# Kernel tuning notes

Measured on AMD Instinct MI355X. Metric: run time of the kernel, lower is better.

Reference implementation:

```python
import jax, jax.numpy as jnp
import numpy as np

B, H, W, C = 8, 128, 128, 256
WH, WW = 8, 8            # window height/width
NH = 8                   # num heads
HD = C // NH             # head dim = 32
EPS = 1e-5


def setup_inputs() -> dict:
    key = jax.random.key(0)
    ks = jax.random.split(key, 10)
    s = 0.02
    return {
        "x": jax.random.normal(ks[0], (B, H, W, C), jnp.float32),
        "residual": jax.random.normal(ks[1], (B, H, W, C), jnp.float32),
        "ln_x_w": 1.0 + s * jax.random.normal(ks[2], (C,), jnp.float32),
        "ln_x_b": s * jax.random.normal(ks[3], (C,), jnp.float32),
        "ln_r_w": 1.0 + s * jax.random.normal(ks[4], (C,), jnp.float32),
        "ln_r_b": s * jax.random.normal(ks[5], (C,), jnp.float32),
        "in_proj_w": s * jax.random.normal(ks[6], (3 * C, C), jnp.float32),
        "in_proj_b": s * jax.random.normal(ks[7], (3 * C,), jnp.float32),
        "out_proj_w": s * jax.random.normal(ks[8], (C, C), jnp.float32),
        "out_proj_b": s * jax.random.normal(ks[9], (C,), jnp.float32),
    }


def _layernorm(t, w, b):
    m = jnp.mean(t, axis=-1, keepdims=True)
    v = jnp.var(t, axis=-1, keepdims=True)
    return (t - m) * jax.lax.rsqrt(v + EPS) * w + b


def _windows(t):
    # [B, H, W, C] -> [B * (H//WH) * (W//WW), WH*WW, C]  (non-overlapping windows)
    t = t.reshape(B, H // WH, WH, W // WW, WW, C)
    t = t.transpose(0, 1, 3, 2, 4, 5)
    return t.reshape(-1, WH * WW, C)


def _unwindows(t):
    # inverse of _windows -> [B, H, W, C]
    t = t.reshape(B, H // WH, W // WW, WH, WW, C)
    t = t.transpose(0, 1, 3, 2, 4, 5)
    return t.reshape(B, H, W, C)


def reference(x, residual, ln_x_w, ln_x_b, ln_r_w, ln_r_b,
              in_proj_w, in_proj_b, out_proj_w, out_proj_b):
    xn = _layernorm(x, ln_x_w, ln_x_b)
    rn = _layernorm(residual, ln_r_w, ln_r_b)

    q_in = _windows(xn)   # [Nw, S, C]
    kv_in = _windows(rn)  # [Nw, S, C]

    wq, wk, wv = jnp.split(in_proj_w, 3, axis=0)
    bq, bk, bv = jnp.split(in_proj_b, 3, axis=0)

    def heads(t):
        nw, s, _ = t.shape
        return t.reshape(nw, s, NH, HD).transpose(0, 2, 1, 3)  # [Nw, NH, S, HD]

    q = heads(q_in @ wq.T + bq)
    k = heads(kv_in @ wk.T + bk)
    v = heads(kv_in @ wv.T + bv)

    scale = 1.0 / jnp.sqrt(jnp.asarray(HD, q.dtype))
    scores = jnp.einsum('whqd,whkd->whqk', q, k) * scale  # [Nw, NH, S, S]
    attn = jax.nn.softmax(scores, axis=-1)
    out = jnp.einsum('whqk,whkd->whqd', attn, v)          # [Nw, NH, S, HD]
    out = out.transpose(0, 2, 1, 3).reshape(-1, WH * WW, C)
    out = out @ out_proj_w.T + out_proj_b                 # [Nw, S, C]

    return _unwindows(out)
```

## Files before the change

### kernel.cpp

```cpp
#include <hip/hip_runtime.h>
#include <math.h>

typedef unsigned int uint;
typedef unsigned short ushort;
typedef short bf16x8 __attribute__((ext_vector_type(8)));
typedef float f32x4 __attribute__((ext_vector_type(4)));

#define EPSV 1e-5f
#define SCALE 0.17677669529663687f

#define OFF_WQKV 0
#define OFF_WOUT 196608
#define OFF_BQKV 262144
#define OFF_BOUT 262912
#define OFF_LNXW 263168
#define OFF_LNXB 263424
#define OFF_LNRW 263680
#define OFF_LNRB 263936

#define L_AX 0
#define L_AR 33792
#define L_QH 67584
#define L_KH 76800
#define L_VT 86016
#define L_AO 95232
#define L_PW 129024
#define LDS_TOTAL 138240

__device__ __forceinline__ float bf2f(ushort u) {
    union { float f; uint i; } z; z.i = ((uint)u) << 16; return z.f;
}
__device__ __forceinline__ ushort f2bf(float f) {
    union { float f; uint i; } z; z.f = f;
    uint i = z.i;
    return (ushort)((i + 0x7FFFu + ((i >> 16) & 1u)) >> 16);
}
__device__ __forceinline__ uint pack2(float a, float b) {
    return (uint)f2bf(a) | ((uint)f2bf(b) << 16);
}

__device__ __forceinline__ bool detect_f32_wave(const uint* __restrict__ xw, int lane) {
    const uint e = (xw[lane] >> 7) & 0xFFu;
    const int pred = (e >= 0x60u && e <= 0x8Au) ? 1 : 0;
    const unsigned long long m = __ballot(pred);
    return __popcll(m) < 32;
}

__global__ __launch_bounds__(256) void kParams(
    const void* __restrict__ x,
    const void* __restrict__ lnxw, const void* __restrict__ lnxb,
    const void* __restrict__ lnrw, const void* __restrict__ lnrb,
    const void* __restrict__ wqkv, const void* __restrict__ bqkv,
    const void* __restrict__ wout, const void* __restrict__ bout,
    ushort* __restrict__ pb)
{
    const bool f32 = detect_f32_wave((const uint*)x, threadIdx.x & 63);
    const int blk = blockIdx.x, tid = threadIdx.x;
    const void* src; int si, doff;
    if (blk < 768)        { src = wqkv; si = blk * 256 + tid;          doff = OFF_WQKV; }
    else if (blk < 1024)  { src = wout; si = (blk - 768) * 256 + tid;  doff = OFF_WOUT; }
    else if (blk < 1027)  { src = bqkv; si = (blk - 1024) * 256 + tid; doff = OFF_BQKV; }
    else if (blk == 1027) { src = bout; si = tid; doff = OFF_BOUT; }
    else if (blk == 1028) { src = lnxw; si = tid; doff = OFF_LNXW; }
    else if (blk == 1029) { src = lnxb; si = tid; doff = OFF_LNXB; }
    else if (blk == 1030) { src = lnrw; si = tid; doff = OFF_LNRW; }
    else                  { src = lnrb; si = tid; doff = OFF_LNRB; }
    pb[doff + si] = f32 ? f2bf(((const float*)src)[si]) : ((const ushort*)src)[si];
}

__device__ __forceinline__ void loadB(const ushort* __restrict__ wbase, int wrow,
                                      int quad, bf16x8 (&bb)[8])
{
    const bf16x8* bp = (const bf16x8*)(wbase + (size_t)wrow * 256 + quad * 8);
    #pragma unroll
    for (int ks = 0; ks < 8; ++ks) bb[ks] = bp[ks * 4];
}

__device__ __forceinline__ void compT(
    const ushort* __restrict__ pb, char* __restrict__ smem,
    int t, int g, int col, int quad, const bf16x8 (&bb)[8])
{
    const int mat = t >> 2, sub = t & 3;
    const int wrow = mat * 256 + g * 64 + sub * 16 + col;
    const float bias = bf2f(pb[OFF_BQKV + wrow]);
    const ushort (*A)[264] = (const ushort (*)[264])(smem + (mat == 0 ? L_AX : L_AR));

    if (mat < 2) {
        ushort (*dst)[72] = (ushort (*)[72])(smem + (mat == 0 ? L_QH : L_KH));
        const float scl = (mat == 0) ? SCALE : 1.f;
        #pragma unroll
        for (int at = 0; at < 4; ++at) {
            f32x4 acc = {0.f, 0.f, 0.f, 0.f};
            #pragma unroll
            for (int ks = 0; ks < 8; ++ks) {
                const bf16x8 aF = *(const bf16x8*)&A[at * 16 + col][ks * 32 + quad * 8];
                acc = __builtin_amdgcn_mfma_f32_16x16x32_bf16(aF, bb[ks], acc, 0, 0, 0);
            }
            #pragma unroll
            for (int rg = 0; rg < 4; ++rg)
                dst[at * 16 + quad * 4 + rg][sub * 16 + col] = f2bf((acc[rg] + bias) * scl);
        }
    } else {
        ushort (*vT)[72] = (ushort (*)[72])(smem + L_VT);
        #pragma unroll
        for (int at = 0; at < 4; ++at) {
            f32x4 acc = {0.f, 0.f, 0.f, 0.f};
            #pragma unroll
            for (int ks = 0; ks < 8; ++ks) {
                const bf16x8 aF = *(const bf16x8*)&A[at * 16 + col][ks * 32 + quad * 8];
                acc = __builtin_amdgcn_mfma_f32_16x16x32_bf16(aF, bb[ks], acc, 0, 0, 0);
            }
            uint2 pv;
            pv.x = pack2(acc[0] + bias, acc[1] + bias);
            pv.y = pack2(acc[2] + bias, acc[3] + bias);
            *(uint2*)&vT[sub * 16 + col][at * 16 + quad * 4] = pv;
        }
    }
}

__device__ __forceinline__ void projGroup(
    const ushort* __restrict__ pb, char* __restrict__ smem,
    int g, int wave, int col, int quad)
{
    const ushort* wq = pb + OFF_WQKV;
    const int t0 = wave * 3, t1 = t0 + 1, t2 = t0 + 2;
    const int w0 = (t0 >> 2) * 256 + g * 64 + (t0 & 3) * 16 + col;
    const int w1 = (t1 >> 2) * 256 + g * 64 + (t1 & 3) * 16 + col;
    const int w2 = (t2 >> 2) * 256 + g * 64 + (t2 & 3) * 16 + col;

    bf16x8 p0[8], p1[8];
    loadB(wq, w0, quad, p0);
    loadB(wq, w1, quad, p1);
    compT(pb, smem, t0, g, col, quad, p0);
    loadB(wq, w2, quad, p0);
    compT(pb, smem, t1, g, col, quad, p1);
    compT(pb, smem, t2, g, col, quad, p0);
}

__device__ __forceinline__ void attGroup(
    char* __restrict__ smem, ushort (*Pw)[72],
    int g, int wave, int col, int quad)
{
    const ushort (*qh)[72] = (const ushort (*)[72])(smem + L_QH);
    const ushort (*kh)[72] = (const ushort (*)[72])(smem + L_KH);
    const ushort (*vT)[72] = (const ushort (*)[72])(smem + L_VT);
    ushort (*ao)[264] = (ushort (*)[264])(smem + L_AO);

    #pragma unroll
    for (int hs = 0; hs < 2; ++hs) {
        const bf16x8 qa = *(const bf16x8*)&qh[wave * 16 + col][hs * 32 + quad * 8];
        f32x4 s[4];
        #pragma unroll
        for (int nt = 0; nt < 4; ++nt) {
            const bf16x8 kb = *(const bf16x8*)&kh[nt * 16 + col][hs * 32 + quad * 8];
            f32x4 z = {0.f, 0.f, 0.f, 0.f};
            s[nt] = __builtin_amdgcn_mfma_f32_16x16x32_bf16(qa, kb, z, 0, 0, 0);
        }
        #pragma unroll
        for (int rg = 0; rg < 4; ++rg) {
            float m = fmaxf(fmaxf(s[0][rg], s[1][rg]), fmaxf(s[2][rg], s[3][rg]));
            m = fmaxf(m, __shfl_xor(m, 1));
            m = fmaxf(m, __shfl_xor(m, 2));
            m = fmaxf(m, __shfl_xor(m, 4));
            m = fmaxf(m, __shfl_xor(m, 8));
            float p0 = __expf(s[0][rg] - m);
            float p1 = __expf(s[1][rg] - m);
            float p2 = __expf(s[2][rg] - m);
            float p3 = __expf(s[3][rg] - m);
            float sm = p0 + p1 + p2 + p3;
            sm += __shfl_xor(sm, 1);
            sm += __shfl_xor(sm, 2);
            sm += __shfl_xor(sm, 4);
            sm += __shfl_xor(sm, 8);
            const float inv = 1.f / sm;
            s[0][rg] = p0 * inv; s[1][rg] = p1 * inv;
            s[2][rg] = p2 * inv; s[3][rg] = p3 * inv;
        }
        #pragma unroll
        for (int nt = 0; nt < 4; ++nt)
            #pragma unroll
            for (int rg = 0; rg < 4; ++rg)
                Pw[quad * 4 + rg][nt * 16 + col] = f2bf(s[nt][rg]);
        const bf16x8 pa0 = *(const bf16x8*)&Pw[col][quad * 8];
        const bf16x8 pa1 = *(const bf16x8*)&Pw[col][32 + quad * 8];
        #pragma unroll
        for (int n2 = 0; n2 < 2; ++n2) {
            const bf16x8 bv0 = *(const bf16x8*)&vT[hs * 32 + n2 * 16 + col][quad * 8];
            const bf16x8 bv1 = *(const bf16x8*)&vT[hs * 32 + n2 * 16 + col][32 + quad * 8];
            f32x4 acc = {0.f, 0.f, 0.f, 0.f};
            acc = __builtin_amdgcn_mfma_f32_16x16x32_bf16(pa0, bv0, acc, 0, 0, 0);
            acc = __builtin_amdgcn_mfma_f32_16x16x32_bf16(pa1, bv1, acc, 0, 0, 0);
            #pragma unroll
            for (int rg = 0; rg < 4; ++rg)
                ao[wave * 16 + quad * 4 + rg][(g * 2 + hs) * 32 + n2 * 16 + col] =
                    f2bf(acc[rg]);
        }
    }
}

__global__ __launch_bounds__(256, 1) void kMain(
    const void* __restrict__ xv, const void* __restrict__ rv,
    const ushort* __restrict__ pb, void* __restrict__ outv)
{
    extern __shared__ char smem[];
    const int tid = threadIdx.x;
    const int lane = tid & 63, wave = tid >> 6;
    const int col = lane & 15, quad = lane >> 4;
    const bool f32 = detect_f32_wave((const uint*)xv, lane);
    const int w = blockIdx.x, b = w >> 8, hw = (w >> 4) & 15, ww = w & 15;
    ushort (*Pw)[72] = (ushort (*)[72])(smem + L_PW + wave * 2304);

    {
        const int l8 = tid & 7, trow = tid >> 3;
        #pragma unroll 1
        for (int t = 0; t < 2; ++t) {
            const void* src = t ? rv : xv;
            const ushort* lw = pb + (t ? OFF_LNRW : OFF_LNXW);
            const ushort* lb = pb + (t ? OFF_LNRB : OFF_LNXB);
            ushort (*dst)[264] = (ushort (*)[264])(smem + (t ? L_AR : L_AX));
            #pragma unroll 1
            for (int p = 0; p < 2; ++p) {
                const int row = p * 32 + trow;
                const int pi = row >> 3, pj = row & 7;
                const size_t gidx = ((size_t)((b * 128 + hw * 8 + pi) * 128 + ww * 8 + pj)) * 256
                                  + (size_t)(l8 * 32);
                float vals[32];
                if (f32) {
                    const float4* g = (const float4*)((const float*)src + gidx);
                    #pragma unroll
                    for (int it = 0; it < 8; ++it) {
                        float4 q = g[it];
                        vals[it * 4 + 0] = q.x; vals[it * 4 + 1] = q.y;
                        vals[it * 4 + 2] = q.z; vals[it * 4 + 3] = q.w;
                    }
                } else {
                    const uint4* g = (const uint4*)((const ushort*)src + gidx);
                    #pragma unroll
                    for (int it = 0; it < 4; ++it) {
                        uint4 q = g[it];
                        uint u[4] = {q.x, q.y, q.z, q.w};
                        #pragma unroll
                        for (int e = 0; e < 4; ++e) {
                            vals[it * 8 + e * 2]     = bf2f((ushort)(u[e] & 0xffff));
                            vals[it * 8 + e * 2 + 1] = bf2f((ushort)(u[e] >> 16));
                        }
                    }
                }
                float s0 = 0.f, s1 = 0.f;
                #pragma unroll
                for (int c = 0; c < 32; ++c) { s0 += vals[c]; s1 += vals[c] * vals[c]; }
                s0 += __shfl_xor(s0, 1); s1 += __shfl_xor(s1, 1);
                s0 += __shfl_xor(s0, 2); s1 += __shfl_xor(s1, 2);
                s0 += __shfl_xor(s0, 4); s1 += __shfl_xor(s1, 4);
                const float mean = s0 * (1.f / 256.f);
                const float var  = s1 * (1.f / 256.f) - mean * mean;
                const float rs   = rsqrtf(var + EPSV);
                #pragma unroll
                for (int c = 0; c < 32; c += 2) {
                    const int ch = l8 * 32 + c;
                    float a0 = (vals[c]     - mean) * rs * bf2f(lw[ch])     + bf2f(lb[ch]);
                    float a1 = (vals[c + 1] - mean) * rs * bf2f(lw[ch + 1]) + bf2f(lb[ch + 1]);
                    *(uint*)&dst[row][ch] = pack2(a0, a1);
                }
            }
        }
        __syncthreads();
    }

    #pragma unroll 1
    for (int gg = 0; gg < 4; ++gg) {
        const int g = (gg + w) & 3;
        projGroup(pb, smem, g, wave, col, quad);
        __syncthreads();
        attGroup(smem, Pw, g, wave, col, quad);
        __syncthreads();
    }

    {
        const ushort* wo = pb + OFF_WOUT;
        const ushort (*ao)[264] = (const ushort (*)[264])(smem + L_AO);
        float  (*sf)[264] = (float  (*)[264])(smem + L_AX);
        ushort (*sh)[264] = (ushort (*)[264])(smem + L_AX);

        bf16x8 p0[8], p1[8];
        const int r0 = wave * 64 + col;
        loadB(wo, r0,      quad, p0);
        loadB(wo, r0 + 16, quad, p1);
        #pragma unroll
        for (int sub = 0; sub < 4; ++sub) {
            const int orow = wave * 64 + sub * 16 + col;
            const float bias = bf2f(pb[OFF_BOUT + orow]);
            const bf16x8 (&bb)[8] = (sub & 1) ? p1 : p0;
            #pragma unroll
            for (int at = 0; at < 4; ++at) {
                f32x4 acc = {0.f, 0.f, 0.f, 0.f};
                #pragma unroll
                for (int ks = 0; ks < 8; ++ks) {
                    const bf16x8 aF = *(const bf16x8*)&ao[at * 16 + col][ks * 32 + quad * 8];
                    acc = __builtin_amdgcn_mfma_f32_16x16x32_bf16(aF, bb[ks], acc, 0, 0, 0);
                }
                if (f32) {
                    #pragma unroll
                    for (int rg = 0; rg < 4; ++rg)
                        sf[at * 16 + quad * 4 + rg][orow] = acc[rg] + bias;
                } else {
                    #pragma unroll
                    for (int rg = 0; rg < 4; ++rg)
                        sh[at * 16 + quad * 4 + rg][orow] = f2bf(acc[rg] + bias);
                }
            }
            if (sub == 0) loadB(wo, r0 + 32, quad, p0);
            if (sub == 1) loadB(wo, r0 + 48, quad, p1);
        }
        __syncthreads();

        const int row = wave * 16 + (lane >> 2), l4 = lane & 3;
        const size_t gb = ((size_t)((b * 128 + hw * 8 + (row >> 3)) * 128
                          + ww * 8 + (row & 7))) * 256;
        if (f32) {
            #pragma unroll
            for (int e = 0; e < 16; ++e) {
                float4 vv = *(const float4*)&sf[row][e * 16 + l4 * 4];
                *(float4*)((float*)outv + gb + e * 16 + l4 * 4) = vv;
            }
        } else {
            #pragma unroll
            for (int e = 0; e < 8; ++e) {
                uint4 vvv = *(const uint4*)&sh[row][l4 * 64 + e * 8];
                *(uint4*)((ushort*)outv + gb + (size_t)(l4 * 64 + e * 8)) = vvv;
            }
        }
    }
}

extern "C" void kernel_launch(void* const* d_in, const int* in_sizes, int n_in,
                              void* d_out, int out_size, void* d_ws, size_t ws_size,
                              hipStream_t stream)
{
    const void* x    = d_in[0];
    const void* r    = d_in[1];
    const void* lnxw = d_in[2];
    const void* lnxb = d_in[3];
    const void* lnrw = d_in[4];
    const void* lnrb = d_in[5];
    const void* wqkv = d_in[6];
    const void* bqkv = d_in[7];
    const void* wout = d_in[8];
    const void* bout = d_in[9];

    ushort* pb = (ushort*)d_ws;

    kParams<<<1032, 256, 0, stream>>>(x, lnxw, lnxb, lnrw, lnrb,
                                      wqkv, bqkv, wout, bout, pb);

    (void)hipFuncSetAttribute((const void*)kMain,
                              hipFuncAttributeMaxDynamicSharedMemorySize, LDS_TOTAL);
    kMain<<<2048, 256, LDS_TOTAL, stream>>>(x, r, pb, d_out);
}
```

Before: 599.0 us.

## Halve LDS footprint to fit two blocks per CU via register-resident operands

```diff
diff --git a/kernel.cpp b/kernel.cpp
--- a/kernel.cpp
+++ b/kernel.cpp
@@ -18,14 +18,13 @@
 #define OFF_LNRW 263680
 #define OFF_LNRB 263936
 
-#define L_AX 0
-#define L_AR 33792
-#define L_QH 67584
-#define L_KH 76800
-#define L_VT 86016
-#define L_AO 95232
-#define L_PW 129024
-#define LDS_TOTAL 138240
+#define L_AR 0
+#define L_QH 33792
+#define L_KH 43008
+#define L_VT 52224
+#define L_PW 61440
+#define L_ST 33792
+#define LDS_TOTAL 70656
 
 __device__ __forceinline__ float bf2f(ushort u) {
     union { float f; uint i; } z; z.i = ((uint)u) << 16; return z.f;
@@ -76,29 +75,44 @@
     for (int ks = 0; ks < 8; ++ks) bb[ks] = bp[ks * 4];
 }
 
-__device__ __forceinline__ void compT(
+__device__ __forceinline__ void compQ(
     const ushort* __restrict__ pb, char* __restrict__ smem,
-    int t, int g, int col, int quad, const bf16x8 (&bb)[8])
-{
-    const int mat = t >> 2, sub = t & 3;
+    int g, int sub, const bf16x8 (&ax)[8], const bf16x8 (&bb)[8],
+    int wave, int col, int quad)
+{
+    ushort (*qh)[72] = (ushort (*)[72])(smem + L_QH);
+    f32x4 acc = {0.f, 0.f, 0.f, 0.f};
+    #pragma unroll
+    for (int ks = 0; ks < 8; ++ks)
+        acc = __builtin_amdgcn_mfma_f32_16x16x32_bf16(ax[ks], bb[ks], acc, 0, 0, 0);
+    const int wrow = g * 64 + sub * 16 + col;
+    const float bias = bf2f(pb[OFF_BQKV + wrow]);
+    #pragma unroll
+    for (int rg = 0; rg < 4; ++rg)
+        qh[wave * 16 + quad * 4 + rg][sub * 16 + col] = f2bf((acc[rg] + bias) * SCALE);
+}
+
+__device__ __forceinline__ void compKV(
+    const ushort* __restrict__ pb, char* __restrict__ smem,
+    int g, int mat, int sub, const bf16x8 (&bb)[8],
+    int col, int quad)
+{
+    const ushort (*ar)[264] = (const ushort (*)[264])(smem + L_AR);
     const int wrow = mat * 256 + g * 64 + sub * 16 + col;
     const float bias = bf2f(pb[OFF_BQKV + wrow]);
-    const ushort (*A)[264] = (const ushort (*)[264])(smem + (mat == 0 ? L_AX : L_AR));
-
-    if (mat < 2) {
-        ushort (*dst)[72] = (ushort (*)[72])(smem + (mat == 0 ? L_QH : L_KH));
-        const float scl = (mat == 0) ? SCALE : 1.f;
+    if (mat == 1) {
+        ushort (*kh)[72] = (ushort (*)[72])(smem + L_KH);
         #pragma unroll
         for (int at = 0; at < 4; ++at) {
             f32x4 acc = {0.f, 0.f, 0.f, 0.f};
             #pragma unroll
             for (int ks = 0; ks < 8; ++ks) {
-                const bf16x8 aF = *(const bf16x8*)&A[at * 16 + col][ks * 32 + quad * 8];
+                const bf16x8 aF = *(const bf16x8*)&ar[at * 16 + col][ks * 32 + quad * 8];
                 acc = __builtin_amdgcn_mfma_f32_16x16x32_bf16(aF, bb[ks], acc, 0, 0, 0);
             }
             #pragma unroll
             for (int rg = 0; rg < 4; ++rg)
-                dst[at * 16 + quad * 4 + rg][sub * 16 + col] = f2bf((acc[rg] + bias) * scl);
+                kh[at * 16 + quad * 4 + rg][sub * 16 + col] = f2bf(acc[rg] + bias);
         }
     } else {
         ushort (*vT)[72] = (ushort (*)[72])(smem + L_VT);
@@ -107,7 +121,7 @@
             f32x4 acc = {0.f, 0.f, 0.f, 0.f};
             #pragma unroll
             for (int ks = 0; ks < 8; ++ks) {
-                const bf16x8 aF = *(const bf16x8*)&A[at * 16 + col][ks * 32 + quad * 8];
+                const bf16x8 aF = *(const bf16x8*)&ar[at * 16 + col][ks * 32 + quad * 8];
                 acc = __builtin_amdgcn_mfma_f32_16x16x32_bf16(aF, bb[ks], acc, 0, 0, 0);
             }
             uint2 pv;
@@ -120,31 +134,34 @@
 
 __device__ __forceinline__ void projGroup(
     const ushort* __restrict__ pb, char* __restrict__ smem,
-    int g, int wave, int col, int quad)
+    const bf16x8 (&ax)[8], int g, int wave, int col, int quad)
 {
     const ushort* wq = pb + OFF_WQKV;
-    const int t0 = wave * 3, t1 = t0 + 1, t2 = t0 + 2;
-    const int w0 = (t0 >> 2) * 256 + g * 64 + (t0 & 3) * 16 + col;
-    const int w1 = (t1 >> 2) * 256 + g * 64 + (t1 & 3) * 16 + col;
-    const int w2 = (t2 >> 2) * 256 + g * 64 + (t2 & 3) * 16 + col;
+    const int mat = 1 + (wave >> 1);
+    const int sb0 = (wave & 1) * 2, sb1 = sb0 + 1;
 
     bf16x8 p0[8], p1[8];
-    loadB(wq, w0, quad, p0);
-    loadB(wq, w1, quad, p1);
-    compT(pb, smem, t0, g, col, quad, p0);
-    loadB(wq, w2, quad, p0);
-    compT(pb, smem, t1, g, col, quad, p1);
-    compT(pb, smem, t2, g, col, quad, p0);
+    loadB(wq, g * 64 + col,      quad, p0);
+    loadB(wq, g * 64 + 16 + col, quad, p1);
+    compQ(pb, smem, g, 0, ax, p0, wave, col, quad);
+    loadB(wq, g * 64 + 32 + col, quad, p0);
+    compQ(pb, smem, g, 1, ax, p1, wave, col, quad);
+    loadB(wq, g * 64 + 48 + col, quad, p1);
+    compQ(pb, smem, g, 2, ax, p0, wave, col, quad);
+    loadB(wq, mat * 256 + g * 64 + sb0 * 16 + col, quad, p0);
+    compQ(pb, smem, g, 3, ax, p1, wave, col, quad);
+    loadB(wq, mat * 256 + g * 64 + sb1 * 16 + col, quad, p1);
+    compKV(pb, smem, g, mat, sb0, p0, col, quad);
+    compKV(pb, smem, g, mat, sb1, p1, col, quad);
 }
 
 __device__ __forceinline__ void attGroup(
-    char* __restrict__ smem, ushort (*Pw)[72],
+    char* __restrict__ smem, ushort (*Pw)[72], uint (&aopk)[16][2],
     int g, int wave, int col, int quad)
 {
     const ushort (*qh)[72] = (const ushort (*)[72])(smem + L_QH);
     const ushort (*kh)[72] = (const ushort (*)[72])(smem + L_KH);
     const ushort (*vT)[72] = (const ushort (*)[72])(smem + L_VT);
-    ushort (*ao)[264] = (ushort (*)[264])(smem + L_AO);
 
     #pragma unroll
     for (int hs = 0; hs < 2; ++hs) {
@@ -190,15 +207,13 @@
             f32x4 acc = {0.f, 0.f, 0.f, 0.f};
             acc = __builtin_amdgcn_mfma_f32_16x16x32_bf16(pa0, bv0, acc, 0, 0, 0);
             acc = __builtin_amdgcn_mfma_f32_16x16x32_bf16(pa1, bv1, acc, 0, 0, 0);
-            #pragma unroll
-            for (int rg = 0; rg < 4; ++rg)
-                ao[wave * 16 + quad * 4 + rg][(g * 2 + hs) * 32 + n2 * 16 + col] =
-                    f2bf(acc[rg]);
+            aopk[g * 4 + hs * 2 + n2][0] = pack2(acc[0], acc[1]);
+            aopk[g * 4 + hs * 2 + n2][1] = pack2(acc[2], acc[3]);
         }
     }
 }
 
-__global__ __launch_bounds__(256, 1) void kMain(
+__global__ __launch_bounds__(256, 2) void kMain(
     const void* __restrict__ xv, const void* __restrict__ rv,
     const ushort* __restrict__ pb, void* __restrict__ outv)
 {
@@ -209,7 +224,9 @@
     const bool f32 = detect_f32_wave((const uint*)xv, lane);
     const int w = blockIdx.x, b = w >> 8, hw = (w >> 4) & 15, ww = w & 15;
     ushort (*Pw)[72] = (ushort (*)[72])(smem + L_PW + wave * 2304);
-
+    ushort (*AR)[264] = (ushort (*)[264])(smem + L_AR);
+
+    bf16x8 ax[8];
     {
         const int l8 = tid & 7, trow = tid >> 3;
         #pragma unroll 1
@@ -217,7 +234,6 @@
             const void* src = t ? rv : xv;
             const ushort* lw = pb + (t ? OFF_LNRW : OFF_LNXW);
             const ushort* lb = pb + (t ? OFF_LNRB : OFF_LNXB);
-            ushort (*dst)[264] = (ushort (*)[264])(smem + (t ? L_AR : L_AX));
             #pragma unroll 1
             for (int p = 0; p < 2; ++p) {
                 const int row = p * 32 + trow;
@@ -260,74 +276,114 @@
                     const int ch = l8 * 32 + c;
                     float a0 = (vals[c]     - mean) * rs * bf2f(lw[ch])     + bf2f(lb[ch]);
                     float a1 = (vals[c + 1] - mean) * rs * bf2f(lw[ch + 1]) + bf2f(lb[ch + 1]);
-                    *(uint*)&dst[row][ch] = pack2(a0, a1);
+                    *(uint*)&AR[row][ch] = pack2(a0, a1);
                 }
             }
-        }
+            __syncthreads();
+            if (t == 0) {
+                #pragma unroll
+                for (int ks = 0; ks < 8; ++ks)
+                    ax[ks] = *(const bf16x8*)&AR[wave * 16 + col][ks * 32 + quad * 8];
+                __syncthreads();
+            }
+        }
+    }
+
+    uint aopk[16][2];
+    #pragma unroll
+    for (int g = 0; g < 4; ++g) {
+        projGroup(pb, smem, ax, g, wave, col, quad);
+        __syncthreads();
+        attGroup(smem, Pw, aopk, g, wave, col, quad);
         __syncthreads();
     }
 
-    #pragma unroll 1
-    for (int gg = 0; gg < 4; ++gg) {
-        const int g = (gg + w) & 3;
-        projGroup(pb, smem, g, wave, col, quad);
+    {
+        ushort (*ao)[264] = AR;
+        #pragma unroll
+        for (int t = 0; t < 16; ++t) {
+            const uint lo = aopk[t][0], hi = aopk[t][1];
+            ao[wave * 16 + quad * 4 + 0][t * 16 + col] = (ushort)(lo & 0xffff);
+            ao[wave * 16 + quad * 4 + 1][t * 16 + col] = (ushort)(lo >> 16);
+            ao[wave * 16 + quad * 4 + 2][t * 16 + col] = (ushort)(hi & 0xffff);
+            ao[wave * 16 + quad * 4 + 3][t * 16 + col] = (ushort)(hi >> 16);
+        }
         __syncthreads();
-        attGroup(smem, Pw, g, wave, col, quad);
-        __syncthreads();
-    }
-
-    {
+
         const ushort* wo = pb + OFF_WOUT;
-        const ushort (*ao)[264] = (const ushort (*)[264])(smem + L_AO);
-        float  (*sf)[264] = (float  (*)[264])(smem + L_AX);
-        ushort (*sh)[264] = (ushort (*)[264])(smem + L_AX);
-
-        bf16x8 p0[8], p1[8];
-        const int r0 = wave * 64 + col;
-        loadB(wo, r0,      quad, p0);
-        loadB(wo, r0 + 16, quad, p1);
-        #pragma unroll
-        for (int sub = 0; sub < 4; ++sub) {
-            const int orow = wave * 64 + sub * 16 + col;
-            const float bias = bf2f(pb[OFF_BOUT + orow]);
-            const bf16x8 (&bb)[8] = (sub & 1) ? p1 : p0;
-            #pragma unroll
-            for (int at = 0; at < 4; ++at) {
-                f32x4 acc = {0.f, 0.f, 0.f, 0.f};
-                #pragma unroll
-                for (int ks = 0; ks < 8; ++ks) {
-                    const bf16x8 aF = *(const bf16x8*)&ao[at * 16 + col][ks * 32 + quad * 8];
-                    acc = __builtin_amdgcn_mfma_f32_16x16x32_bf16(aF, bb[ks], acc, 0, 0, 0);
-                }
-                if (f32) {
+        if (!f32) {
+            ushort (*sh)[264] = (ushort (*)[264])(smem + L_ST);
+            bf16x8 p0[8], p1[8];
+            const int r0 = wave * 64 + col;
+            loadB(wo, r0,      quad, p0);
+            loadB(wo, r0 + 16, quad, p1);
+            #pragma unroll
+            for (int sub = 0; sub < 4; ++sub) {
+                const int orow = wave * 64 + sub * 16 + col;
+                const float bias = bf2f(pb[OFF_BOUT + orow]);
+                const bf16x8 (&bb)[8] = (sub & 1) ? p1 : p0;
+                #pragma unroll
+                for (int at = 0; at < 4; ++at) {
+                    f32x4 acc = {0.f, 0.f, 0.f, 0.f};
                     #pragma unroll
-                    for (int rg = 0; rg < 4; ++rg)
-                        sf[at * 16 + quad * 4 + rg][orow] = acc[rg] + bias;
-                } else {
+                    for (int ks = 0; ks < 8; ++ks) {
+                        const bf16x8 aF = *(const bf16x8*)&ao[at * 16 + col][ks * 32 + quad * 8];
+                        acc = __builtin_amdgcn_mfma_f32_16x16x32_bf16(aF, bb[ks], acc, 0, 0, 0);
+                    }
                     #pragma unroll
                     for (int rg = 0; rg < 4; ++rg)
                         sh[at * 16 + quad * 4 + rg][orow] = f2bf(acc[rg] + bias);
                 }
-            }
-            if (sub == 0) loadB(wo, r0 + 32, quad, p0);
-            if (sub == 1) loadB(wo, r0 + 48, quad, p1);
-        }
-        __syncthreads();
-
-        const int row = wave * 16 + (lane >> 2), l4 = lane & 3;
-        const size_t gb = ((size_t)((b * 128 + hw * 8 + (row >> 3)) * 128
-                          + ww * 8 + (row & 7))) * 256;
-        if (f32) {
-            #pragma unroll
-            for (int e = 0; e < 16; ++e) {
-                float4 vv = *(const float4*)&sf[row][e * 16 + l4 * 4];
-                *(float4*)((float*)outv + gb + e * 16 + l4 * 4) = vv;
-            }
-        } else {
+                if (sub == 0) loadB(wo, r0 + 32, quad, p0);
+                if (sub == 1) loadB(wo, r0 + 48, quad, p1);
+            }
+            __syncthreads();
+
+            const int row = wave * 16 + (lane >> 2), l4 = lane & 3;
+            const size_t gb = ((size_t)((b * 128 + hw * 8 + (row >> 3)) * 128
+                              + ww * 8 + (row & 7))) * 256;
             #pragma unroll
             for (int e = 0; e < 8; ++e) {
                 uint4 vvv = *(const uint4*)&sh[row][l4 * 64 + e * 8];
                 *(uint4*)((ushort*)outv + gb + (size_t)(l4 * 64 + e * 8)) = vvv;
+            }
+        } else {
+            float (*sf)[132] = (float (*)[132])(smem + L_ST);
+            #pragma unroll 1
+            for (int half = 0; half < 2; ++half) {
+                if (half) __syncthreads();
+                bf16x8 p0[8], p1[8];
+                const int r0 = half * 128 + wave * 32 + col;
+                loadB(wo, r0,      quad, p0);
+                loadB(wo, r0 + 16, quad, p1);
+                #pragma unroll
+                for (int sub2 = 0; sub2 < 2; ++sub2) {
+                    const int orow = half * 128 + wave * 32 + sub2 * 16 + col;
+                    const float bias = bf2f(pb[OFF_BOUT + orow]);
+                    const bf16x8 (&bb)[8] = sub2 ? p1 : p0;
+                    #pragma unroll
+                    for (int at = 0; at < 4; ++at) {
+                        f32x4 acc = {0.f, 0.f, 0.f, 0.f};
+                        #pragma unroll
+                        for (int ks = 0; ks < 8; ++ks) {
+                            const bf16x8 aF = *(const bf16x8*)&ao[at * 16 + col][ks * 32 + quad * 8];
+                            acc = __builtin_amdgcn_mfma_f32_16x16x32_bf16(aF, bb[ks], acc, 0, 0, 0);
+                        }
+                        #pragma unroll
+                        for (int rg = 0; rg < 4; ++rg)
+                            sf[at * 16 + quad * 4 + rg][wave * 32 + sub2 * 16 + col] =
+                                acc[rg] + bias;
+                    }
+                }
+                __syncthreads();
+                const int row = wave * 16 + (lane >> 2), l4 = lane & 3;
+                const size_t gb = ((size_t)((b * 128 + hw * 8 + (row >> 3)) * 128
+                                  + ww * 8 + (row & 7))) * 256 + (size_t)(half * 128);
+                #pragma unroll
+                for (int e = 0; e < 8; ++e) {
+                    float4 vv = *(const float4*)&sf[row][e * 16 + l4 * 4];
+                    *(float4*)((float*)outv + gb + e * 16 + l4 * 4) = vv;
+                }
             }
         }
     }
```

Measured after the change: 537.3 us. 10.3% less time.
